# Optimization experiments

Measured on AMD Instinct MI355X. Metric: run time of the kernel, lower is better.

## Reference

```python
import jax, jax.numpy as jnp
import numpy as np

N_WAY = 100
K_SHOT = 10
N_SUPPORT = N_WAY * K_SHOT
N_QUERY = 8192
F_IN = 4096
D_EMB = 1024
EPS = 1e-6  # torch nn.PairwiseDistance default eps added to the difference


def setup_inputs() -> dict:
    key = jax.random.key(0)
    k1, k2, k3, k4 = jax.random.split(key, 4)
    support_images = jax.random.normal(k1, (N_SUPPORT, F_IN), dtype=jnp.float32)
    # dense labels 0..N_WAY-1, K_SHOT examples each (episodic sampling)
    support_labels = (jnp.arange(N_SUPPORT, dtype=jnp.int32) // K_SHOT)
    query_images = jax.random.normal(k2, (N_QUERY, F_IN), dtype=jnp.float32)
    W = jax.random.normal(k3, (F_IN, D_EMB), dtype=jnp.float32) * (1.0 / np.sqrt(F_IN))
    b = jax.random.normal(k4, (D_EMB,), dtype=jnp.float32) * 0.01
    return {"support_images": support_images, "support_labels": support_labels,
            "query_images": query_images, "W": W, "b": b}


def reference(support_images, support_labels, query_images, W, b):
    # backbone: linear feature extractor
    z_support = support_images @ W + b          # [N_SUPPORT, D]
    z_query = query_images @ W + b              # [N_QUERY, D]

    # group support embeddings by class (each class has exactly K_SHOT members)
    order = jnp.argsort(support_labels, stable=True)
    grouped = z_support[order].reshape(N_WAY, K_SHOT, D_EMB)  # [W, K, D]

    # torch .median(dim=0): lower median for even counts -> sorted[(K-1)//2]
    z_proto_med = jnp.sort(grouped, axis=1)[:, (K_SHOT - 1) // 2]  # [W, D]
    z_proto_mean = grouped.mean(axis=1)                            # [W, D]
    z_total = 0.5 * (z_proto_med + z_proto_mean)                   # [W, D]

    # pairwise L2 with torch PairwiseDistance eps: sqrt(sum((q - p + eps)^2))
    # expanded: ||q||^2 + ||p||^2 + D*eps^2 - 2 q.p + 2*eps*(sum q - sum p)
    q2 = jnp.sum(z_query * z_query, axis=-1, keepdims=True)       # [Q, 1]
    p2 = jnp.sum(z_total * z_total, axis=-1)[None, :]             # [1, W]
    qs = jnp.sum(z_query, axis=-1, keepdims=True)                 # [Q, 1]
    ps = jnp.sum(z_total, axis=-1)[None, :]                       # [1, W]
    cross = z_query @ z_total.T                                   # [Q, W]
    sq = q2 + p2 - 2.0 * cross + 2.0 * EPS * (qs - ps) + D_EMB * EPS * EPS
    dists = jnp.sqrt(jnp.maximum(sq, 0.0))                        # [Q, W]
    return -dists
```

## Files before the change

kernel.cpp:

```cpp
#include <hip/hip_runtime.h>


typedef unsigned short u16;
typedef __attribute__((ext_vector_type(4))) unsigned short u16x4;
typedef __attribute__((ext_vector_type(8))) unsigned short u16x8;
typedef __attribute__((ext_vector_type(8))) short bf16x8;
typedef __attribute__((ext_vector_type(4))) float f32x4;

#define N_QUERY 8192
#define F_IN    4096
#define D_EMB   1024
#define N_SUP   1000
#define N_WAY   100
#define BK      64

__device__ __forceinline__ u16 f2b(float f) {
  unsigned int u = __builtin_bit_cast(unsigned int, f);
  u += 0x7FFFu + ((u >> 16) & 1u);
  return (u16)(u >> 16);
}

#define GLB_PTR(p) ((const __attribute__((address_space(1))) unsigned int*)(p))
#define LDS_PTR(p) ((__attribute__((address_space(3))) unsigned int*)(p))

__global__ __launch_bounds__(256) void wt_k(const float* __restrict__ W,
                                            u16* __restrict__ Wt) {
  __shared__ float tile[32][33];
  int kb = blockIdx.x * 32, nb = blockIdx.y * 32;
  int tx = threadIdx.x & 31, ty = threadIdx.x >> 5;
#pragma unroll
  for (int i = 0; i < 4; ++i) {
    int k = ty + i * 8;
    tile[k][tx] = W[(size_t)(kb + k) * D_EMB + nb + tx];
  }
  __syncthreads();
#pragma unroll
  for (int i = 0; i < 4; ++i) {
    int n = ty + i * 8;
    Wt[(size_t)(nb + n) * F_IN + kb + tx] = f2b(tile[tx][n]);
  }
}

__global__ __launch_bounds__(256) void gemm1_k(
    const float* __restrict__ qimg, const float* __restrict__ simg,
    const u16* __restrict__ Wt, const float* __restrict__ bias,
    float* __restrict__ Z) {
  __shared__ __align__(16) u16 As[64 * BK];
  __shared__ __align__(16) u16 Bs[128 * BK];
  const int tid  = threadIdx.x;
  const int lane = tid & 63, wid = tid >> 6;
  const int wr = wid >> 1, wc = wid & 1;
  int lin = blockIdx.x + (blockIdx.y << 3);
  int swz = (lin & 7) * 144 + (lin >> 3);
  const int rowBase = (swz >> 3) * 64;
  const int colBase = (swz & 7) * 128;

  const float* asrc[2];
  int aw[2];
#pragma unroll
  for (int i = 0; i < 2; ++i) {
    int g = i * 256 + tid;
    int row = g >> 3;
    int colb = ((g & 7) << 4) ^ ((row & 7) << 4);
    int grow = rowBase + row;
    int sr = grow - N_QUERY; if (sr < 0) sr = 0; if (sr > N_SUP - 1) sr = N_SUP - 1;
    const float* base = (grow < N_QUERY) ? qimg + (size_t)grow * F_IN
                                         : simg + (size_t)sr * F_IN;
    asrc[i] = base + (colb >> 1);
    aw[i] = g * 8;
  }
  const u16* bsrc[4];
  unsigned bldsoff[4];
#pragma unroll
  for (int i = 0; i < 4; ++i) {
    int g = i * 256 + tid;
    int n = g >> 3;
    int kb = ((g & 7) << 4) ^ ((n & 7) << 4);
    bsrc[i] = Wt + (size_t)(colBase + n) * F_IN + (kb >> 1);
    bldsoff[i] = i * 4096 + wid * 1024;
  }
  int aoff[2], boff[4];
#pragma unroll
  for (int m = 0; m < 2; ++m) {
    int row = wr * 32 + m * 16 + (lane & 15);
    aoff[m] = (row * 128 + (((lane >> 4) << 4) ^ ((row & 7) << 4))) >> 1;
  }
#pragma unroll
  for (int n = 0; n < 4; ++n) {
    int row = wc * 64 + n * 16 + (lane & 15);
    boff[n] = (row * 128 + (((lane >> 4) << 4) ^ ((row & 7) << 4))) >> 1;
  }

  f32x4 acc[2][4] = {};

#pragma unroll 1
  for (int kt = 0; kt < F_IN / BK; ++kt) {
    const float* p0 = asrc[0] + kt * BK;
    const float* p1 = asrc[1] + kt * BK;
    float4 v00 = *(const float4*)p0, v01 = *(const float4*)(p0 + 4);
    float4 v10 = *(const float4*)p1, v11 = *(const float4*)(p1 + 4);
#pragma unroll
    for (int i = 0; i < 4; ++i)
      __builtin_amdgcn_global_load_lds(GLB_PTR(bsrc[i] + kt * BK),
                                       LDS_PTR((char*)Bs + bldsoff[i]), 16, 0, 0);
    u16x8 pk0 = { f2b(v00.x), f2b(v00.y), f2b(v00.z), f2b(v00.w),
                  f2b(v01.x), f2b(v01.y), f2b(v01.z), f2b(v01.w) };
    u16x8 pk1 = { f2b(v10.x), f2b(v10.y), f2b(v10.z), f2b(v10.w),
                  f2b(v11.x), f2b(v11.y), f2b(v11.z), f2b(v11.w) };
    *(u16x8*)&As[aw[0]] = pk0;
    *(u16x8*)&As[aw[1]] = pk1;
    __syncthreads();

#pragma unroll
    for (int ks = 0; ks < 2; ++ks) {
      bf16x8 a[2], b[4];
#pragma unroll
      for (int m = 0; m < 2; ++m) a[m] = *(const bf16x8*)&As[aoff[m] ^ (ks << 5)];
#pragma unroll
      for (int n = 0; n < 4; ++n) b[n] = *(const bf16x8*)&Bs[boff[n] ^ (ks << 5)];
#pragma unroll
      for (int m = 0; m < 2; ++m)
#pragma unroll
        for (int n = 0; n < 4; ++n)
          acc[m][n] = __builtin_amdgcn_mfma_f32_16x16x32_bf16(a[m], b[n], acc[m][n], 0, 0, 0);
    }
    __syncthreads();
  }

#pragma unroll
  for (int n = 0; n < 4; ++n) {
    int c = colBase + wc * 64 + n * 16 + (lane & 15);
    float bvv = bias[c];
#pragma unroll
    for (int m = 0; m < 2; ++m) {
      int r0 = rowBase + wr * 32 + m * 16 + ((lane >> 4) * 4);
#pragma unroll
      for (int r = 0; r < 4; ++r)
        Z[(size_t)(r0 + r) * D_EMB + c] = acc[m][n][r] + bvv;
    }
  }
}

__global__ __launch_bounds__(256) void proto_k(const float* __restrict__ Z,
                                               float* __restrict__ Ztf) {
  int gid = blockIdx.x * 256 + threadIdx.x;
  int w = gid >> 10, d = gid & 1023;
  float outv = 0.f;
  if (w < N_WAY) {
    float v[10]; float s = 0.f;
#pragma unroll
    for (int k = 0; k < 10; ++k) {
      v[k] = Z[(size_t)(N_QUERY + w * 10 + k) * D_EMB + d];
      s += v[k];
    }
#pragma unroll
    for (int a = 0; a < 9; ++a)
#pragma unroll
      for (int b2 = 0; b2 < 9; ++b2)
        if (b2 < 9 - a) {
          float lo = fminf(v[b2], v[b2 + 1]);
          float hi = fmaxf(v[b2], v[b2 + 1]);
          v[b2] = lo; v[b2 + 1] = hi;
        }
    outv = 0.5f * (v[4] + s * 0.1f);
  }
  Ztf[gid] = outv;
}

__global__ __launch_bounds__(256) void stats_k(const float* __restrict__ in,
                                               u16* __restrict__ outb,
                                               float* __restrict__ sum2,
                                               float* __restrict__ sum1) {
  int row = blockIdx.x;
  const float* r = in + (size_t)row * D_EMB;
  int t = threadIdx.x;
  float4 v = *(const float4*)(r + t * 4);
  u16x4 u4 = { f2b(v.x), f2b(v.y), f2b(v.z), f2b(v.w) };
  *(u16x4*)(outb + (size_t)row * D_EMB + t * 4) = u4;
  float s  = v.x + v.y + v.z + v.w;
  float s2 = v.x * v.x + v.y * v.y + v.z * v.z + v.w * v.w;
#pragma unroll
  for (int off = 32; off > 0; off >>= 1) {
    s  += __shfl_down(s, off);
    s2 += __shfl_down(s2, off);
  }
  __shared__ float as1[4], as2[4];
  if ((t & 63) == 0) { as1[t >> 6] = s; as2[t >> 6] = s2; }
  __syncthreads();
  if (t == 0) {
    sum1[row] = as1[0] + as1[1] + as1[2] + as1[3];
    sum2[row] = as2[0] + as2[1] + as2[2] + as2[3];
  }
}

#define LDA2 40
__global__ __launch_bounds__(256) void gemm2_k(
    const u16* __restrict__ Zq, const u16* __restrict__ Ztb,
    const float* __restrict__ q2, const float* __restrict__ qs,
    const float* __restrict__ p2, const float* __restrict__ ps,
    float* __restrict__ out) {
  __shared__ u16 As[64][LDA2];
  __shared__ u16 Bs[128][LDA2];
  const int tid = threadIdx.x;
  const int lane = tid & 63, wid = tid >> 6;
  const int wr = wid >> 1, wc = wid & 1;
  const int rowBase = blockIdx.x * 64;

  f32x4 acc[2][4] = {};

  for (int kt = 0; kt < D_EMB / 32; ++kt) {
    u16x8 avv;
    {
      int row = tid >> 2, kh = tid & 3;
      avv = *(const u16x8*)(Zq + (size_t)(rowBase + row) * D_EMB + kt * 32 + kh * 8);
    }
    u16x8 bvv[2];
#pragma unroll
    for (int i = 0; i < 2; ++i) {
      int u = i * 256 + tid;
      int n = u >> 2, kh = u & 3;
      bvv[i] = *(const u16x8*)(Ztb + (size_t)n * D_EMB + kt * 32 + kh * 8);
    }
    __syncthreads();
    {
      int row = tid >> 2, kh = tid & 3;
      *(u16x8*)&As[row][kh * 8] = avv;
    }
#pragma unroll
    for (int i = 0; i < 2; ++i) {
      int u = i * 256 + tid;
      int n = u >> 2, kh = u & 3;
      *(u16x8*)&Bs[n][kh * 8] = bvv[i];
    }
    __syncthreads();

    bf16x8 a[2], b[4];
#pragma unroll
    for (int m = 0; m < 2; ++m)
      a[m] = *(const bf16x8*)&As[wr * 32 + m * 16 + (lane & 15)][(lane >> 4) * 8];
#pragma unroll
    for (int n = 0; n < 4; ++n)
      b[n] = *(const bf16x8*)&Bs[wc * 64 + n * 16 + (lane & 15)][(lane >> 4) * 8];
#pragma unroll
    for (int m = 0; m < 2; ++m)
#pragma unroll
      for (int n = 0; n < 4; ++n)
        acc[m][n] = __builtin_amdgcn_mfma_f32_16x16x32_bf16(a[m], b[n], acc[m][n], 0, 0, 0);
    __syncthreads();
  }

#pragma unroll
  for (int m = 0; m < 2; ++m) {
    int r0 = rowBase + wr * 32 + m * 16 + ((lane >> 4) * 4);
    float q2v[4], qsv[4];
#pragma unroll
    for (int r = 0; r < 4; ++r) { q2v[r] = q2[r0 + r]; qsv[r] = qs[r0 + r]; }
#pragma unroll
    for (int n = 0; n < 4; ++n) {
      int c = wc * 64 + n * 16 + (lane & 15);
      if (c < N_WAY) {
        float pp = p2[c], pss = ps[c];
#pragma unroll
        for (int r = 0; r < 4; ++r) {
          float sq = q2v[r] + pp - 2.f * acc[m][n][r]
                   + 2e-6f * (qsv[r] - pss) + (float)D_EMB * 1e-12f;
          out[(size_t)(r0 + r) * N_WAY + c] = -sqrtf(fmaxf(sq, 0.f));
        }
      }
    }
  }
}

extern "C" void kernel_launch(void* const* d_in, const int* in_sizes, int n_in,
                              void* d_out, int out_size, void* d_ws, size_t ws_size,
                              hipStream_t stream) {
  const float* simg = (const float*)d_in[0];
  const float* qimg = (const float*)d_in[2];
  const float* W    = (const float*)d_in[3];
  const float* bias = (const float*)d_in[4];
  float* out = (float*)d_out;

  char* ws = (char*)d_ws;
  u16*   Wt  = (u16*)(ws);
  float* Z   = (float*)(ws + 8388608);
  u16*   Zq  = (u16*)(ws + 46137344);
  float* Ztf = (float*)(ws + 62914560);
  u16*   Ztb = (u16*)(ws + 63438848);
  float* q2  = (float*)(ws + 63700992);
  float* qs  = (float*)(ws + 63733760);
  float* p2  = (float*)(ws + 63766528);
  float* ps  = (float*)(ws + 63767040);

  hipLaunchKernelGGL(wt_k,    dim3(128, 32), dim3(256), 0, stream, W, Wt);
  hipLaunchKernelGGL(gemm1_k, dim3(8, 144),  dim3(256), 0, stream, qimg, simg, Wt, bias, Z);
  hipLaunchKernelGGL(proto_k, dim3(512),     dim3(256), 0, stream, Z, Ztf);
  hipLaunchKernelGGL(stats_k, dim3(8192),    dim3(256), 0, stream, Z, Zq, q2, qs);
  hipLaunchKernelGGL(stats_k, dim3(128),     dim3(256), 0, stream, Ztf, Ztb, p2, ps);
  hipLaunchKernelGGL(gemm2_k, dim3(128),     dim3(256), 0, stream, Zq, Ztb, q2, qs, p2, ps, out);
}
```

Measured before the change: 170.4 us.

## Write bf16 embeddings directly from first GEMM and drop fp32 intermediate

```diff
diff --git a/kernel.cpp b/kernel.cpp
--- a/kernel.cpp
+++ b/kernel.cpp
@@ -19,6 +19,10 @@
   u += 0x7FFFu + ((u >> 16) & 1u);
   return (u16)(u >> 16);
 }
+__device__ __forceinline__ float b2f(u16 u) {
+  unsigned int x = ((unsigned int)u) << 16;
+  return __builtin_bit_cast(float, x);
+}
 
 #define GLB_PTR(p) ((const __attribute__((address_space(1))) unsigned int*)(p))
 #define LDS_PTR(p) ((__attribute__((address_space(3))) unsigned int*)(p))
@@ -44,16 +48,14 @@
 __global__ __launch_bounds__(256) void gemm1_k(
     const float* __restrict__ qimg, const float* __restrict__ simg,
     const u16* __restrict__ Wt, const float* __restrict__ bias,
-    float* __restrict__ Z) {
+    u16* __restrict__ Zq) {
   __shared__ __align__(16) u16 As[64 * BK];
   __shared__ __align__(16) u16 Bs[128 * BK];
   const int tid  = threadIdx.x;
   const int lane = tid & 63, wid = tid >> 6;
   const int wr = wid >> 1, wc = wid & 1;
-  int lin = blockIdx.x + (blockIdx.y << 3);
-  int swz = (lin & 7) * 144 + (lin >> 3);
-  const int rowBase = (swz >> 3) * 64;
-  const int colBase = (swz & 7) * 128;
+  const int rowBase = blockIdx.y * 64;
+  const int colBase = blockIdx.x * 128;
 
   const float* asrc[2];
   int aw[2];
@@ -136,12 +138,12 @@
       int r0 = rowBase + wr * 32 + m * 16 + ((lane >> 4) * 4);
 #pragma unroll
       for (int r = 0; r < 4; ++r)
-        Z[(size_t)(r0 + r) * D_EMB + c] = acc[m][n][r] + bvv;
-    }
-  }
-}
-
-__global__ __launch_bounds__(256) void proto_k(const float* __restrict__ Z,
+        Zq[(size_t)(r0 + r) * D_EMB + c] = f2b(acc[m][n][r] + bvv);
+    }
+  }
+}
+
+__global__ __launch_bounds__(256) void proto_k(const u16* __restrict__ Zq,
                                                float* __restrict__ Ztf) {
   int gid = blockIdx.x * 256 + threadIdx.x;
   int w = gid >> 10, d = gid & 1023;
@@ -150,7 +152,7 @@
     float v[10]; float s = 0.f;
 #pragma unroll
     for (int k = 0; k < 10; ++k) {
-      v[k] = Z[(size_t)(N_QUERY + w * 10 + k) * D_EMB + d];
+      v[k] = b2f(Zq[(size_t)(N_QUERY + w * 10 + k) * D_EMB + d]);
       s += v[k];
     }
 #pragma unroll
@@ -165,6 +167,29 @@
     outv = 0.5f * (v[4] + s * 0.1f);
   }
   Ztf[gid] = outv;
+}
+
+__global__ __launch_bounds__(256) void statsq_k(const u16* __restrict__ Zq,
+                                                float* __restrict__ sum2,
+                                                float* __restrict__ sum1) {
+  int row = blockIdx.x;
+  int t = threadIdx.x;
+  u16x4 u = *(const u16x4*)(Zq + (size_t)row * D_EMB + t * 4);
+  float x0 = b2f(u[0]), x1 = b2f(u[1]), x2 = b2f(u[2]), x3 = b2f(u[3]);
+  float s  = x0 + x1 + x2 + x3;
+  float s2 = x0 * x0 + x1 * x1 + x2 * x2 + x3 * x3;
+#pragma unroll
+  for (int o = 32; o > 0; o >>= 1) {
+    s  += __shfl_down(s, o);
+    s2 += __shfl_down(s2, o);
+  }
+  __shared__ float as1[4], as2[4];
+  if ((t & 63) == 0) { as1[t >> 6] = s; as2[t >> 6] = s2; }
+  __syncthreads();
+  if (t == 0) {
+    sum1[row] = as1[0] + as1[1] + as1[2] + as1[3];
+    sum2[row] = as2[0] + as2[1] + as2[2] + as2[3];
+  }
 }
 
 __global__ __launch_bounds__(256) void stats_k(const float* __restrict__ in,
@@ -282,19 +307,18 @@
 
   char* ws = (char*)d_ws;
   u16*   Wt  = (u16*)(ws);
-  float* Z   = (float*)(ws + 8388608);
-  u16*   Zq  = (u16*)(ws + 46137344);
-  float* Ztf = (float*)(ws + 62914560);
-  u16*   Ztb = (u16*)(ws + 63438848);
-  float* q2  = (float*)(ws + 63700992);
-  float* qs  = (float*)(ws + 63733760);
-  float* p2  = (float*)(ws + 63766528);
-  float* ps  = (float*)(ws + 63767040);
+  u16*   Zq  = (u16*)(ws + 8388608);
+  float* Ztf = (float*)(ws + 27262976);
+  u16*   Ztb = (u16*)(ws + 27787264);
+  float* q2  = (float*)(ws + 28049408);
+  float* qs  = (float*)(ws + 28082176);
+  float* p2  = (float*)(ws + 28114944);
+  float* ps  = (float*)(ws + 28115456);
 
   hipLaunchKernelGGL(wt_k,    dim3(128, 32), dim3(256), 0, stream, W, Wt);
-  hipLaunchKernelGGL(gemm1_k, dim3(8, 144),  dim3(256), 0, stream, qimg, simg, Wt, bias, Z);
-  hipLaunchKernelGGL(proto_k, dim3(512),     dim3(256), 0, stream, Z, Ztf);
-  hipLaunchKernelGGL(stats_k, dim3(8192),    dim3(256), 0, stream, Z, Zq, q2, qs);
+  hipLaunchKernelGGL(gemm1_k, dim3(8, 144),  dim3(256), 0, stream, qimg, simg, Wt, bias, Zq);
+  hipLaunchKernelGGL(proto_k, dim3(512),     dim3(256), 0, stream, Zq, Ztf);
+  hipLaunchKernelGGL(statsq_k, dim3(8192),   dim3(256), 0, stream, Zq, q2, qs);
   hipLaunchKernelGGL(stats_k, dim3(128),     dim3(256), 0, stream, Ztf, Ztb, p2, ps);
   hipLaunchKernelGGL(gemm2_k, dim3(128),     dim3(256), 0, stream, Zq, Ztb, q2, qs, p2, ps, out);
 }
```

Result: slower. 233.5 us (+37.0%).
